# Optimization experiments

Measured on AMD Instinct MI355X. Metric: run time of the kernel, lower is better.

Reference implementation:

```python
import jax, jax.numpy as jnp
import numpy as np

F = 128
NRBF = 20
CUTOFF = 5.0
L = 3
NZ = 100
F2 = F // 2
N = 10000
E = 256000
NMOL = 100
EPS = 1e-8


def setup_inputs() -> dict:
    key = jax.random.key(0)
    ks = jax.random.split(key, 20)
    xyz = jax.random.uniform(ks[0], (N, 3), jnp.float32) * 10.0
    z = jax.random.randint(ks[1], (N,), 0, NZ)
    nbrs = jax.random.randint(ks[2], (E, 2), 0, N)
    # avoid self-edges (would give zero distance in the sinc RBF)
    nbrs = nbrs.at[:, 1].set(jnp.where(nbrs[:, 1] == nbrs[:, 0], (nbrs[:, 1] + 1) % N, nbrs[:, 1]))
    mol_idx = jnp.sort(jax.random.randint(ks[3], (N,), 0, NMOL))

    def p(k, shape, scale=0.05):
        return jax.random.normal(k, shape, jnp.float32) * scale

    return dict(
        xyz=xyz, z=z, nbrs=nbrs, mol_idx=mol_idx,
        emb=p(ks[4], (NZ, F), 1.0),
        msg_W1=p(ks[5], (L, F, F)), msg_b1=jnp.zeros((L, F), jnp.float32),
        msg_W2=p(ks[6], (L, F, 3 * F)), msg_b2=jnp.zeros((L, 3 * F), jnp.float32),
        dist_W=p(ks[7], (L, NRBF, 3 * F)), dist_b=jnp.zeros((L, 3 * F), jnp.float32),
        upd_U=p(ks[8], (L, F, F)), upd_V=p(ks[9], (L, F, F)),
        upd_W1=p(ks[10], (L, 2 * F, F)), upd_b1=jnp.zeros((L, F), jnp.float32),
        upd_W2=p(ks[11], (L, F, 3 * F)), upd_b2=jnp.zeros((L, 3 * F), jnp.float32),
        read_W1=p(ks[12], (F, F2)), read_b1=jnp.zeros((F2,), jnp.float32),
        read_W2=p(ks[13], (F2, 1)), read_b2=jnp.zeros((1,), jnp.float32),
    )


def _painn(xyz, emb, msg_W1, msg_b1, msg_W2, msg_b2, dist_W, dist_b,
           upd_U, upd_V, upd_W1, upd_b1, upd_W2, upd_b2,
           read_W1, read_b1, read_W2, read_b2, z, nbrs, mol_idx):
    idx_i = nbrs[:, 0]
    idx_j = nbrs[:, 1]
    r_ij = xyz[idx_j] - xyz[idx_i]                       # [E,3]
    d = jnp.sqrt(jnp.sum(r_ij * r_ij, -1) + EPS)          # [E]
    unit = r_ij / d[:, None]
    # sinc radial basis + cosine cutoff envelope
    nvec = jnp.arange(1, NRBF + 1, dtype=xyz.dtype)
    rbf = jnp.sin(nvec[None, :] * jnp.pi * d[:, None] / CUTOFF) / d[:, None]   # [E,NRBF]
    fcut = 0.5 * (jnp.cos(jnp.pi * d / CUTOFF) + 1.0) * (d < CUTOFF)           # [E]

    s_i = emb[z]                                          # [N,F]
    v_i = jnp.zeros((xyz.shape[0], F, 3), xyz.dtype)      # [N,F,3]

    for l in range(L):
        # message block: invariant filter on nodes, gather to edges
        phi = (jax.nn.silu(s_i @ msg_W1[l] + msg_b1[l]) @ msg_W2[l] + msg_b2[l])[idx_j]  # [E,3F]
        w_s = (rbf @ dist_W[l] + dist_b[l]) * fcut[:, None]                               # [E,3F]
        inv = (phi * w_s).reshape(-1, 3, F)
        ds_edge = inv[:, 0]                                                               # [E,F]
        dv_edge = inv[:, 1][:, :, None] * v_i[idx_j] + inv[:, 2][:, :, None] * unit[:, None, :]  # [E,F,3]
        s_i = s_i + jax.ops.segment_sum(ds_edge, idx_i, num_segments=s_i.shape[0])
        v_i = v_i + jax.ops.segment_sum(dv_edge, idx_i, num_segments=s_i.shape[0])

        # update block: channel-mixing of vectors + gated scalar/vector residuals
        u_v = jnp.einsum('nfv,fg->ngv', v_i, upd_U[l])
        v_v = jnp.einsum('nfv,fg->ngv', v_i, upd_V[l])
        vnorm = jnp.sqrt(jnp.sum(v_v * v_v, -1) + EPS)                                    # [N,F]
        a = (jax.nn.silu(jnp.concatenate([s_i, vnorm], -1) @ upd_W1[l] + upd_b1[l])
             @ upd_W2[l] + upd_b2[l]).reshape(-1, 3, F)
        dv = u_v * a[:, 0][:, :, None]
        ds = a[:, 1] * jnp.sum(u_v * v_v, -1) + a[:, 2]
        s_i = s_i + ds
        v_i = v_i + dv

    atom_e = jax.nn.silu(s_i @ read_W1 + read_b1) @ read_W2 + read_b2                     # [N,1]
    energy = jax.ops.segment_sum(atom_e[:, 0], mol_idx, num_segments=NMOL)                # [NMOL]
    return energy


def reference(xyz, z, nbrs, mol_idx, emb, msg_W1, msg_b1, msg_W2, msg_b2,
              dist_W, dist_b, upd_U, upd_V, upd_W1, upd_b1, upd_W2, upd_b2,
              read_W1, read_b1, read_W2, read_b2):
    return _painn(xyz, emb, msg_W1, msg_b1, msg_W2, msg_b2, dist_W, dist_b,
                  upd_U, upd_V, upd_W1, upd_b1, upd_W2, upd_b2,
                  read_W1, read_b1, read_W2, read_b2, z, nbrs, mol_idx)
```

## Files before the change

### kernel.cpp

```cpp
#include <hip/hip_runtime.h>
#include <hip/hip_bf16.h>
#include <math.h>

#define NA 10000
#define NE 256000
#define FDIM 128
#define F3 384
#define NRBF 20
#define NLAYERS 3
#define NMOLS 100
#define CAP 96
#define WROW 388
#define PACK_BLOCKS 2288
#define CUTOFF_F 5.0f
#define EPS_F 1e-8f
#define PI_F 3.14159265358979323846f

typedef __attribute__((ext_vector_type(8))) short bf16x8;
typedef __attribute__((ext_vector_type(4))) float f32x4;

struct pv6 { unsigned int u0, u1, u2; };

__device__ __forceinline__ float silu_f(float x) { return x / (1.0f + __expf(-x)); }

__device__ __forceinline__ unsigned short f2bf(float x) {
  unsigned u = __float_as_uint(x);
  return (unsigned short)((u + 0x7FFFu + ((u >> 16) & 1u)) >> 16);
}
__device__ __forceinline__ float bf2f(unsigned short u) {
  return __uint_as_float(((unsigned)u) << 16);
}
__device__ __forceinline__ float lo_f(unsigned int u) { return bf2f((unsigned short)(u & 0xFFFFu)); }
__device__ __forceinline__ float hi_f(unsigned int u) { return bf2f((unsigned short)(u >> 16)); }

__device__ __forceinline__ void pack_one(const float* __restrict__ src,
                                         unsigned short* __restrict__ dst,
                                         int loc, int per, int N) {
  int lay = loc / per;
  int kn = loc - lay * per;
  int k = kn / N, n = kn - k * N;
  int kb = k >> 5, q = (k >> 3) & 3, j = k & 7, nt = n >> 4, c = n & 15;
  int NT = N >> 4;
  dst[(size_t)lay * per + (((kb * NT + nt) * 64 + (q * 16 + c)) * 8 + j)] = f2bf(src[loc]);
}

__device__ __forceinline__ void pack_dw(const float* __restrict__ dW,
                                        const float* __restrict__ db,
                                        unsigned short* __restrict__ dst, int loc) {
  int lay = loc / 12288;
  int kn = loc - lay * 12288;
  int k = kn / 384, n = kn - k * 384;
  float val = 0.0f;
  if (k < NRBF) val = dW[lay * NRBF * 384 + k * 384 + n];
  else if (k == NRBF) val = db[lay * 384 + n];
  int q = (k >> 3) & 3, j = k & 7, nt = n >> 4, c = n & 15;
  dst[(size_t)lay * 12288 + ((nt * 64 + (q * 16 + c)) * 8 + j)] = f2bf(val);
}

__global__ __launch_bounds__(256) void prep_kernel(
    const float* __restrict__ msgW1, const float* __restrict__ msgW2,
    const float* __restrict__ updU, const float* __restrict__ updV,
    const float* __restrict__ updW1, const float* __restrict__ updW2,
    const float* __restrict__ rW1, const float* __restrict__ distW,
    const float* __restrict__ distb, unsigned short* __restrict__ dst,
    const float* __restrict__ xyz, const int* __restrict__ nbrs,
    float* __restrict__ unitv, unsigned short* __restrict__ rbf_bf,
    float* __restrict__ fcut,
    int* __restrict__ deg, int* __restrict__ slot_e, int* __restrict__ slot_j) {
  int b = blockIdx.x;
  if (b < PACK_BLOCKS) {
    int t = b * 256 + threadIdx.x;
    if (t < 49152) pack_one(msgW1, dst, t, 16384, 128);
    else if (t < 196608) pack_one(msgW2, dst + 49152, t - 49152, 49152, 384);
    else if (t < 245760) pack_one(updU, dst + 196608, t - 196608, 16384, 128);
    else if (t < 294912) pack_one(updV, dst + 245760, t - 245760, 16384, 128);
    else if (t < 393216) pack_one(updW1, dst + 294912, t - 294912, 32768, 128);
    else if (t < 540672) pack_one(updW2, dst + 393216, t - 393216, 49152, 384);
    else if (t < 548864) pack_one(rW1, dst + 540672, t - 540672, 8192, 64);
    else if (t < 585728) pack_dw(distW, distb, dst + 548864, t - 548864);
    return;
  }
  int e = (b - PACK_BLOCKS) * 256 + threadIdx.x;
  if (e >= NE) return;
  int i = nbrs[2 * e + 0], j = nbrs[2 * e + 1];
  float rx = xyz[3 * j + 0] - xyz[3 * i + 0];
  float ry = xyz[3 * j + 1] - xyz[3 * i + 1];
  float rz = xyz[3 * j + 2] - xyz[3 * i + 2];
  float d = sqrtf(rx * rx + ry * ry + rz * rz + EPS_F);
  if (d >= CUTOFF_F) return;
  float invd = 1.0f / d;
  float fc = 0.5f * (__cosf(PI_F * d / CUTOFF_F) + 1.0f);
  unitv[3 * e + 0] = rx * invd;
  unitv[3 * e + 1] = ry * invd;
  unitv[3 * e + 2] = rz * invd;
  fcut[e] = fc;
  float base = PI_F * d / CUTOFF_F;
  float sc = invd * fc;
#pragma unroll
  for (int k = 0; k < NRBF; k++)
    rbf_bf[(size_t)e * NRBF + k] = f2bf(__sinf((float)(k + 1) * base) * sc);
  int pos = atomicAdd(&deg[i], 1);
  if (pos < CAP) {
    slot_e[i * CAP + pos] = e;
    slot_j[i * CAP + pos] = j;
  }
}

__global__ __launch_bounds__(256) void msg0_mfma_kernel(
    const float* __restrict__ emb, const int* __restrict__ z, float* __restrict__ s_out,
    const unsigned short* __restrict__ pW1, const float* __restrict__ b1,
    const unsigned short* __restrict__ pW2, const float* __restrict__ b2,
    pv6* __restrict__ cmb) {
  __shared__ bf16x8 sA[4 * 64];
  __shared__ bf16x8 hA[4 * 64];
  int a0 = blockIdx.x * 16;
  int t = threadIdx.x;
  int lane = t & 63, w = t >> 6;
  {
    int kb = t >> 6, l = t & 63;
    int m = l & 15, q = l >> 4;
    int zi = z[a0 + m];
    const float* sp = emb + (size_t)zi * FDIM + kb * 32 + q * 8;
    float* so = s_out + (size_t)(a0 + m) * FDIM + kb * 32 + q * 8;
    bf16x8 c;
#pragma unroll
    for (int j = 0; j < 8; j++) {
      float v = sp[j];
      so[j] = v;
      c[j] = (short)f2bf(v);
    }
    sA[kb * 64 + l] = c;
  }
  __syncthreads();
  f32x4 accH[2];
#pragma unroll
  for (int t2 = 0; t2 < 2; t2++)
#pragma unroll
    for (int r = 0; r < 4; r++) accH[t2][r] = 0.0f;
  const bf16x8* W1f = (const bf16x8*)pW1;
#pragma unroll
  for (int kb = 0; kb < 4; kb++) {
    bf16x8 a = sA[kb * 64 + lane];
#pragma unroll
    for (int t2 = 0; t2 < 2; t2++) {
      bf16x8 b = W1f[(kb * 8 + 2 * w + t2) * 64 + lane];
      accH[t2] = __builtin_amdgcn_mfma_f32_16x16x32_bf16(a, b, accH[t2], 0, 0, 0);
    }
  }
  short* hs = (short*)hA;
#pragma unroll
  for (int t2 = 0; t2 < 2; t2++) {
    int n = w * 32 + t2 * 16 + (lane & 15);
    int kb = n >> 5, q = (n >> 3) & 3, j = n & 7;
    float bias = b1[n];
#pragma unroll
    for (int r = 0; r < 4; r++) {
      int m = (lane >> 4) * 4 + r;
      hs[(kb * 64 + q * 16 + m) * 8 + j] = (short)f2bf(silu_f(accH[t2][r] + bias));
    }
  }
  __syncthreads();
  f32x4 accP[3][2];
#pragma unroll
  for (int c3 = 0; c3 < 3; c3++)
#pragma unroll
    for (int t2 = 0; t2 < 2; t2++)
#pragma unroll
      for (int r = 0; r < 4; r++) accP[c3][t2][r] = 0.0f;
  const bf16x8* W2f = (const bf16x8*)pW2;
#pragma unroll
  for (int kb = 0; kb < 4; kb++) {
    bf16x8 a = hA[kb * 64 + lane];
#pragma unroll
    for (int c3 = 0; c3 < 3; c3++)
#pragma unroll
      for (int t2 = 0; t2 < 2; t2++) {
        bf16x8 b = W2f[(kb * 24 + c3 * 8 + 2 * w + t2) * 64 + lane];
        accP[c3][t2] = __builtin_amdgcn_mfma_f32_16x16x32_bf16(a, b, accP[c3][t2], 0, 0, 0);
      }
  }
#pragma unroll
  for (int t2 = 0; t2 < 2; t2++) {
    int g = (2 * w + t2) * 16 + (lane & 15);
    float bb0 = b2[g], bb1 = b2[FDIM + g], bb2 = b2[2 * FDIM + g];
#pragma unroll
    for (int r = 0; r < 4; r++) {
      int m = (lane >> 4) * 4 + r;
      unsigned p0 = f2bf(accP[0][t2][r] + bb0);
      unsigned p1 = f2bf(accP[1][t2][r] + bb1);
      unsigned p2 = f2bf(accP[2][t2][r] + bb2);
      pv6 rec;
      rec.u0 = p0 | (p1 << 16);
      rec.u1 = p2;
      rec.u2 = 0;
      cmb[(size_t)(a0 + m) * FDIM + g] = rec;
    }
  }
}

__global__ __launch_bounds__(128) void edge_kernel(
    const pv6* __restrict__ cmb, unsigned short* __restrict__ v_lin,
    float* __restrict__ s, const unsigned short* __restrict__ pDW,
    const int* __restrict__ deg, const int* __restrict__ slot_e,
    const int* __restrict__ slot_j, const unsigned short* __restrict__ rbf_bf,
    const float* __restrict__ fcut, const float* __restrict__ unitv) {
  __shared__ bf16x8 aLDS[64];
  __shared__ unsigned short w_lds[16][WROW];
  __shared__ float l_u[16][3];
  __shared__ int l_j[16];
  int i = blockIdx.x;
  int t = threadIdx.x;
  int f = t;
  int lane = t & 63, w = t >> 6;
  int cnt = deg[i];
  if (cnt > CAP) cnt = CAP;
  int base = i * CAP;
  float acc_s = 0.f, av0 = 0.f, av1 = 0.f, av2 = 0.f;
  const bf16x8* Bf = (const bf16x8*)pDW;
  for (int c0 = 0; c0 < cnt; c0 += 16) {
    int ccnt = cnt - c0;
    if (ccnt > 16) ccnt = 16;
    __syncthreads();
    if (t < 64) {
      int m = t & 15, q = t >> 4;
      bf16x8 a;
#pragma unroll
      for (int j = 0; j < 8; j++) a[j] = 0;
      int p = c0 + m;
      if (p < cnt) {
        int e = slot_e[base + p];
        const unsigned short* rb = rbf_bf + (size_t)e * NRBF;
#pragma unroll
        for (int j = 0; j < 8; j++) {
          int k = q * 8 + j;
          if (k < NRBF) a[j] = (short)rb[k];
          else if (k == NRBF) a[j] = (short)f2bf(fcut[e]);
        }
      }
      aLDS[t] = a;
    } else if (t < 80) {
      int idx = t - 64;
      int p = c0 + idx;
      if (p < cnt) {
        int e = slot_e[base + p];
        l_j[idx] = slot_j[base + p];
        l_u[idx][0] = unitv[3 * e + 0];
        l_u[idx][1] = unitv[3 * e + 1];
        l_u[idx][2] = unitv[3 * e + 2];
      }
    }
    __syncthreads();
    {
      bf16x8 a = aLDS[lane];
      int n0 = lane & 15, m0 = (lane >> 4) * 4;
#pragma unroll
      for (int tt = 0; tt < 12; tt++) {
        int nt = 12 * w + tt;
        f32x4 acc;
#pragma unroll
        for (int r = 0; r < 4; r++) acc[r] = 0.0f;
        acc = __builtin_amdgcn_mfma_f32_16x16x32_bf16(a, Bf[nt * 64 + lane], acc, 0, 0, 0);
        int n = nt * 16 + n0;
#pragma unroll
        for (int r = 0; r < 4; r++) w_lds[m0 + r][n] = f2bf(acc[r]);
      }
    }
    __syncthreads();
    int pp = 0;
    for (; pp + 4 <= ccnt; pp += 4) {
      pv6 R[4];
#pragma unroll
      for (int u = 0; u < 4; u++) R[u] = cmb[(size_t)l_j[pp + u] * FDIM + f];
#pragma unroll
      for (int u = 0; u < 4; u++) {
        float p0 = lo_f(R[u].u0), p1 = hi_f(R[u].u0), p2 = lo_f(R[u].u1);
        float v0 = hi_f(R[u].u1), v1 = lo_f(R[u].u2), v2 = hi_f(R[u].u2);
        float w0 = bf2f(w_lds[pp + u][f]), w1 = bf2f(w_lds[pp + u][FDIM + f]),
              w2 = bf2f(w_lds[pp + u][2 * FDIM + f]);
        acc_s += p0 * w0;
        float i1 = p1 * w1, i2 = p2 * w2;
        av0 += i1 * v0 + i2 * l_u[pp + u][0];
        av1 += i1 * v1 + i2 * l_u[pp + u][1];
        av2 += i1 * v2 + i2 * l_u[pp + u][2];
      }
    }
    for (; pp < ccnt; pp++) {
      pv6 R0 = cmb[(size_t)l_j[pp] * FDIM + f];
      float p0 = lo_f(R0.u0), p1 = hi_f(R0.u0), p2 = lo_f(R0.u1);
      float v0 = hi_f(R0.u1), v1 = lo_f(R0.u2), v2 = hi_f(R0.u2);
      float w0 = bf2f(w_lds[pp][f]), w1 = bf2f(w_lds[pp][FDIM + f]),
            w2 = bf2f(w_lds[pp][2 * FDIM + f]);
      acc_s += p0 * w0;
      float i1 = p1 * w1, i2 = p2 * w2;
      av0 += i1 * v0 + i2 * l_u[pp][0];
      av1 += i1 * v1 + i2 * l_u[pp][1];
      av2 += i1 * v2 + i2 * l_u[pp][2];
    }
  }
  {
    pv6 RI = cmb[(size_t)i * FDIM + f];
    av0 += hi_f(RI.u1);
    av1 += lo_f(RI.u2);
    av2 += hi_f(RI.u2);
  }
  unsigned short* vlo = v_lin + (size_t)i * F3;
  vlo[f] = f2bf(av0);
  vlo[FDIM + f] = f2bf(av1);
  vlo[2 * FDIM + f] = f2bf(av2);
  s[(size_t)i * FDIM + f] += acc_s;
}

__global__ __launch_bounds__(256) void upd_fused_kernel(
    float* __restrict__ s, const unsigned short* __restrict__ v_lin,
    pv6* __restrict__ cmb,
    const unsigned short* __restrict__ pU, const unsigned short* __restrict__ pV,
    const unsigned short* __restrict__ pW1, const float* __restrict__ b1,
    const unsigned short* __restrict__ pW2, const float* __restrict__ b2,
    int mode,
    const unsigned short* __restrict__ pMW1, const float* __restrict__ mb1,
    const unsigned short* __restrict__ pMW2, const float* __restrict__ mb2,
    const unsigned short* __restrict__ pRW1, const float* __restrict__ rb1,
    const float* __restrict__ rW2, const float* __restrict__ rb2,
    float* __restrict__ atom_e) {
  __shared__ bf16x8 vAf[3 * 4 * 64];
  __shared__ bf16x8 catA[8 * 64];
  __shared__ bf16x8 hA[4 * 64];
  __shared__ float red[4][16];
  int a0 = blockIdx.x * 16;
  int t = threadIdx.x;
  int lane = t & 63, w = t >> 6;
  {
    int l = t & 63, kb = (t >> 6) & 3;
    int m = l & 15, q = l >> 4;
#pragma unroll
    for (int rt = 0; rt < 3; rt++) {
      vAf[(rt * 4 + kb) * 64 + l] =
          *(const bf16x8*)(v_lin + (size_t)(a0 + m) * F3 + rt * FDIM + kb * 32 + q * 8);
    }
    const float* sp = s + (size_t)(a0 + m) * FDIM + kb * 32 + q * 8;
    bf16x8 c;
#pragma unroll
    for (int j = 0; j < 8; j++) c[j] = (short)f2bf(sp[j]);
    catA[kb * 64 + l] = c;
  }
  __syncthreads();
  f32x4 accU[3][2], accV[3][2];
#pragma unroll
  for (int rt = 0; rt < 3; rt++)
#pragma unroll
    for (int t2 = 0; t2 < 2; t2++)
#pragma unroll
      for (int r = 0; r < 4; r++) { accU[rt][t2][r] = 0.0f; accV[rt][t2][r] = 0.0f; }
  const bf16x8* Uf = (const bf16x8*)pU;
  const bf16x8* Vf = (const bf16x8*)pV;
#pragma unroll
  for (int kb = 0; kb < 4; kb++) {
    bf16x8 bu[2], bv[2];
#pragma unroll
    for (int t2 = 0; t2 < 2; t2++) {
      bu[t2] = Uf[(kb * 8 + 2 * w + t2) * 64 + lane];
      bv[t2] = Vf[(kb * 8 + 2 * w + t2) * 64 + lane];
    }
#pragma unroll
    for (int rt = 0; rt < 3; rt++) {
      bf16x8 a = vAf[(rt * 4 + kb) * 64 + lane];
#pragma unroll
      for (int t2 = 0; t2 < 2; t2++) {
        accU[rt][t2] = __builtin_amdgcn_mfma_f32_16x16x32_bf16(a, bu[t2], accU[rt][t2], 0, 0, 0);
        accV[rt][t2] = __builtin_amdgcn_mfma_f32_16x16x32_bf16(a, bv[t2], accV[rt][t2], 0, 0, 0);
      }
    }
  }
  short* cs = (short*)catA;
#pragma unroll
  for (int t2 = 0; t2 < 2; t2++) {
    int g = w * 32 + t2 * 16 + (lane & 15);
    int k = 128 + g;
    int kb = k >> 5, q = (k >> 3) & 3, j = k & 7;
#pragma unroll
    for (int r = 0; r < 4; r++) {
      int m = (lane >> 4) * 4 + r;
      float x0 = accV[0][t2][r], x1 = accV[1][t2][r], x2 = accV[2][t2][r];
      cs[(kb * 64 + q * 16 + m) * 8 + j] = (short)f2bf(sqrtf(x0 * x0 + x1 * x1 + x2 * x2 + EPS_F));
    }
  }
  __syncthreads();
  f32x4 accH[2];
#pragma unroll
  for (int t2 = 0; t2 < 2; t2++)
#pragma unroll
    for (int r = 0; r < 4; r++) accH[t2][r] = 0.0f;
  const bf16x8* W1f = (const bf16x8*)pW1;
#pragma unroll
  for (int kb = 0; kb < 8; kb++) {
    bf16x8 a = catA[kb * 64 + lane];
#pragma unroll
    for (int t2 = 0; t2 < 2; t2++) {
      bf16x8 b = W1f[(kb * 8 + 2 * w + t2) * 64 + lane];
      accH[t2] = __builtin_amdgcn_mfma_f32_16x16x32_bf16(a, b, accH[t2], 0, 0, 0);
    }
  }
  short* hs = (short*)hA;
#pragma unroll
  for (int t2 = 0; t2 < 2; t2++) {
    int n = w * 32 + t2 * 16 + (lane & 15);
    int kb = n >> 5, q = (n >> 3) & 3, j = n & 7;
    float bias = b1[n];
#pragma unroll
    for (int r = 0; r < 4; r++) {
      int m = (lane >> 4) * 4 + r;
      hs[(kb * 64 + q * 16 + m) * 8 + j] = (short)f2bf(silu_f(accH[t2][r] + bias));
    }
  }
  __syncthreads();
  f32x4 accA[3][2];
#pragma unroll
  for (int c3 = 0; c3 < 3; c3++)
#pragma unroll
    for (int t2 = 0; t2 < 2; t2++)
#pragma unroll
      for (int r = 0; r < 4; r++) accA[c3][t2][r] = 0.0f;
  const bf16x8* W2f = (const bf16x8*)pW2;
#pragma unroll
  for (int kb = 0; kb < 4; kb++) {
    bf16x8 a = hA[kb * 64 + lane];
#pragma unroll
    for (int c3 = 0; c3 < 3; c3++)
#pragma unroll
      for (int t2 = 0; t2 < 2; t2++) {
        bf16x8 b = W2f[(kb * 24 + c3 * 8 + 2 * w + t2) * 64 + lane];
        accA[c3][t2] = __builtin_amdgcn_mfma_f32_16x16x32_bf16(a, b, accA[c3][t2], 0, 0, 0);
      }
  }
  const short* vls = (const short*)vAf;
  unsigned short v0keep[2][4];
#pragma unroll
  for (int t2 = 0; t2 < 2; t2++) {
    int g = w * 32 + t2 * 16 + (lane & 15);
    float bb0 = b2[g], bb1 = b2[FDIM + g], bb2 = b2[2 * FDIM + g];
    int kb = g >> 5, q = (g >> 3) & 3, j = g & 7;
#pragma unroll
    for (int r = 0; r < 4; r++) {
      int m = (lane >> 4) * 4 + r;
      int n = a0 + m;
      float a0v = accA[0][t2][r] + bb0;
      float a1v = accA[1][t2][r] + bb1;
      float a2v = accA[2][t2][r] + bb2;
      float dot = accU[0][t2][r] * accV[0][t2][r] + accU[1][t2][r] * accV[1][t2][r] +
                  accU[2][t2][r] * accV[2][t2][r];
      float s_new = s[(size_t)n * FDIM + g] + a1v * dot + a2v;
      if (mode == 0) {
        s[(size_t)n * FDIM + g] = s_new;
        float nv[3];
#pragma unroll
        for (int c = 0; c < 3; c++) {
          float vold = bf2f((unsigned short)vls[(((c * 4 + kb) * 64) + (q * 16 + m)) * 8 + j]);
          nv[c] = vold + a0v * accU[c][t2][r];
        }
        v0keep[t2][r] = f2bf(nv[0]);
        cmb[(size_t)n * FDIM + g].u2 = (unsigned)f2bf(nv[1]) | ((unsigned)f2bf(nv[2]) << 16);
      }
      cs[(kb * 64 + q * 16 + m) * 8 + j] = (short)f2bf(s_new);
    }
  }
  __syncthreads();
  if (mode == 0) {
    f32x4 accH2[2];
#pragma unroll
    for (int t2 = 0; t2 < 2; t2++)
#pragma unroll
      for (int r = 0; r < 4; r++) accH2[t2][r] = 0.0f;
    const bf16x8* MW1f = (const bf16x8*)pMW1;
#pragma unroll
    for (int kb = 0; kb < 4; kb++) {
      bf16x8 a = catA[kb * 64 + lane];
#pragma unroll
      for (int t2 = 0; t2 < 2; t2++) {
        bf16x8 b = MW1f[(kb * 8 + 2 * w + t2) * 64 + lane];
        accH2[t2] = __builtin_amdgcn_mfma_f32_16x16x32_bf16(a, b, accH2[t2], 0, 0, 0);
      }
    }
#pragma unroll
    for (int t2 = 0; t2 < 2; t2++) {
      int n = w * 32 + t2 * 16 + (lane & 15);
      int kb = n >> 5, q = (n >> 3) & 3, j = n & 7;
      float bias = mb1[n];
#pragma unroll
      for (int r = 0; r < 4; r++) {
        int m = (lane >> 4) * 4 + r;
        hs[(kb * 64 + q * 16 + m) * 8 + j] = (short)f2bf(silu_f(accH2[t2][r] + bias));
      }
    }
    __syncthreads();
    f32x4 accP[3][2];
#pragma unroll
    for (int c3 = 0; c3 < 3; c3++)
#pragma unroll
      for (int t2 = 0; t2 < 2; t2++)
#pragma unroll
        for (int r = 0; r < 4; r++) accP[c3][t2][r] = 0.0f;
    const bf16x8* MW2f = (const bf16x8*)pMW2;
#pragma unroll
    for (int kb = 0; kb < 4; kb++) {
      bf16x8 a = hA[kb * 64 + lane];
#pragma unroll
      for (int c3 = 0; c3 < 3; c3++)
#pragma unroll
        for (int t2 = 0; t2 < 2; t2++) {
          bf16x8 b = MW2f[(kb * 24 + c3 * 8 + 2 * w + t2) * 64 + lane];
          accP[c3][t2] = __builtin_amdgcn_mfma_f32_16x16x32_bf16(a, b, accP[c3][t2], 0, 0, 0);
        }
    }
#pragma unroll
    for (int t2 = 0; t2 < 2; t2++) {
      int g = (2 * w + t2) * 16 + (lane & 15);
      float bb0 = mb2[g], bb1 = mb2[FDIM + g], bb2v = mb2[2 * FDIM + g];
#pragma unroll
      for (int r = 0; r < 4; r++) {
        int m = (lane >> 4) * 4 + r;
        unsigned p0 = f2bf(accP[0][t2][r] + bb0);
        unsigned p1 = f2bf(accP[1][t2][r] + bb1);
        unsigned p2 = f2bf(accP[2][t2][r] + bb2v);
        pv6* rec = &cmb[(size_t)(a0 + m) * FDIM + g];
        rec->u0 = p0 | (p1 << 16);
        rec->u1 = p2 | ((unsigned)v0keep[t2][r] << 16);
      }
    }
  } else {
    f32x4 acc;
#pragma unroll
    for (int r = 0; r < 4; r++) acc[r] = 0.0f;
    const bf16x8* RW1f = (const bf16x8*)pRW1;
#pragma unroll
    for (int kb = 0; kb < 4; kb++) {
      bf16x8 a = catA[kb * 64 + lane];
      bf16x8 b = RW1f[(kb * 4 + w) * 64 + lane];
      acc = __builtin_amdgcn_mfma_f32_16x16x32_bf16(a, b, acc, 0, 0, 0);
    }
    int col = w * 16 + (lane & 15);
    float bias = rb1[col], w2v = rW2[col];
    float val[4];
#pragma unroll
    for (int r = 0; r < 4; r++) val[r] = silu_f(acc[r] + bias) * w2v;
#pragma unroll
    for (int off = 1; off < 16; off <<= 1)
#pragma unroll
      for (int r = 0; r < 4; r++) val[r] += __shfl_xor(val[r], off, 64);
    if ((lane & 15) == 0) {
#pragma unroll
      for (int r = 0; r < 4; r++) red[w][(lane >> 4) * 4 + r] = val[r];
    }
    __syncthreads();
    if (t < 16) {
      atom_e[a0 + t] = red[0][t] + red[1][t] + red[2][t] + red[3][t] + rb2[0];
    }
  }
}

__global__ __launch_bounds__(256) void mol_reduce_kernel(
    const float* __restrict__ atom_e, const int* __restrict__ mol_idx,
    float* __restrict__ out) {
  __shared__ float molsum[NMOLS];
  int t = threadIdx.x;
  if (t < NMOLS) molsum[t] = 0.0f;
  __syncthreads();
  int n = blockIdx.x * 256 + t;
  if (n < NA) atomicAdd(&molsum[mol_idx[n]], atom_e[n]);
  __syncthreads();
  if (t < NMOLS && molsum[t] != 0.0f) atomicAdd(&out[t], molsum[t]);
}

extern "C" void kernel_launch(void* const* d_in, const int* in_sizes, int n_in,
                              void* d_out, int out_size, void* d_ws, size_t ws_size,
                              hipStream_t stream) {
  const float* xyz = (const float*)d_in[0];
  const int* z = (const int*)d_in[1];
  const int* nbrs = (const int*)d_in[2];
  const int* mol = (const int*)d_in[3];
  const float* emb = (const float*)d_in[4];
  const float* msgW1 = (const float*)d_in[5];
  const float* msgb1 = (const float*)d_in[6];
  const float* msgW2 = (const float*)d_in[7];
  const float* msgb2 = (const float*)d_in[8];
  const float* distW = (const float*)d_in[9];
  const float* distb = (const float*)d_in[10];
  const float* updU = (const float*)d_in[11];
  const float* updV = (const float*)d_in[12];
  const float* updW1 = (const float*)d_in[13];
  const float* updb1 = (const float*)d_in[14];
  const float* updW2 = (const float*)d_in[15];
  const float* updb2 = (const float*)d_in[16];
  const float* rW1 = (const float*)d_in[17];
  const float* rb1 = (const float*)d_in[18];
  const float* rW2 = (const float*)d_in[19];
  const float* rb2 = (const float*)d_in[20];

  float* ws = (float*)d_ws;
  float* s = ws;      ws += (size_t)NA * FDIM;
  float* fcut = ws;   ws += (size_t)NE;
  float* unitv = ws;  ws += (size_t)NE * 3;
  float* atom_e = ws; ws += (size_t)NA;
  int* deg = (int*)ws;
  int* slot_e = deg + NA;
  int* slot_j = slot_e + NA * CAP;
  unsigned short* pk = (unsigned short*)(((uintptr_t)(slot_j + NA * CAP) + 15) & ~(uintptr_t)15);
  unsigned short* pMsgW1 = pk;
  unsigned short* pMsgW2 = pMsgW1 + 49152;
  unsigned short* pUpdU  = pMsgW2 + 147456;
  unsigned short* pUpdV  = pUpdU + 49152;
  unsigned short* pUpdW1 = pUpdV + 49152;
  unsigned short* pUpdW2 = pUpdW1 + 98304;
  unsigned short* pRW1   = pUpdW2 + 147456;
  unsigned short* pDW    = pRW1 + 8192;
  unsigned short* rbf_bf = (unsigned short*)(((uintptr_t)(pDW + 36864) + 15) & ~(uintptr_t)15);
  unsigned short* after_rbf = rbf_bf + (size_t)NE * NRBF + 8;
  pv6* cmb = (pv6*)(((uintptr_t)after_rbf + 15) & ~(uintptr_t)15);
  unsigned short* v_lin = (unsigned short*)(cmb + (size_t)NA * FDIM);

  hipMemsetAsync(deg, 0, NA * sizeof(int), stream);
  hipMemsetAsync(d_out, 0, NMOLS * sizeof(float), stream);

  prep_kernel<<<PACK_BLOCKS + NE / 256, 256, 0, stream>>>(
      msgW1, msgW2, updU, updV, updW1, updW2, rW1, distW, distb, pMsgW1,
      xyz, nbrs, unitv, rbf_bf, fcut, deg, slot_e, slot_j);
  msg0_mfma_kernel<<<NA / 16, 256, 0, stream>>>(emb, z, s, pMsgW1, msgb1, pMsgW2, msgb2, cmb);

  for (int l = 0; l < NLAYERS; l++) {
    edge_kernel<<<NA, 128, 0, stream>>>(cmb, v_lin, s,
                                        pDW + (size_t)l * 12288,
                                        deg, slot_e, slot_j, rbf_bf, fcut, unitv);
    int mode = (l == NLAYERS - 1) ? 1 : 0;
    int lnext = (l + 1 < NLAYERS) ? l + 1 : 0;
    upd_fused_kernel<<<NA / 16, 256, 0, stream>>>(
        s, v_lin, cmb, pUpdU + (size_t)l * 16384, pUpdV + (size_t)l * 16384,
        pUpdW1 + (size_t)l * 32768, updb1 + (size_t)l * FDIM,
        pUpdW2 + (size_t)l * 49152, updb2 + (size_t)l * F3,
        mode,
        pMsgW1 + (size_t)lnext * 16384, msgb1 + (size_t)lnext * FDIM,
        pMsgW2 + (size_t)lnext * 49152, msgb2 + (size_t)lnext * F3,
        pRW1, rb1, rW2, rb2, atom_e);
  }
  mol_reduce_kernel<<<(NA + 255) / 256, 256, 0, stream>>>(atom_e, mol, (float*)d_out);
}
```

Measured before the change: 298.9 us.

## Prefetch neighbor gathers across MFMA stage and cut barriers in edge kernel

The edge kernel now preloads all slot edge and neighbor indices into LDS once per atom. For each 16-edge chunk it issues all 16 neighbor record gathers up front, so they overlap the RBF MFMA that builds the filter weights. Each wave builds its own MFMA A-operand in registers instead of staging it through LDS, and the full __syncthreads calls are replaced by an lgkmcnt-wait plus s_barrier. The cost is more registers (16 pv6 records per thread), which the added launch bound of 4 has to accommodate, with some risk of spilling.

After: 402.2 us. +34.6%, slower.

```diff
diff --git a/kernel.cpp b/kernel.cpp
--- a/kernel.cpp
+++ b/kernel.cpp
@@ -32,6 +32,11 @@
 }
 __device__ __forceinline__ float lo_f(unsigned int u) { return bf2f((unsigned short)(u & 0xFFFFu)); }
 __device__ __forceinline__ float hi_f(unsigned int u) { return bf2f((unsigned short)(u >> 16)); }
+
+__device__ __forceinline__ void bar_lds() {
+  asm volatile("s_waitcnt lgkmcnt(0)" ::: "memory");
+  __builtin_amdgcn_s_barrier();
+}
 
 __device__ __forceinline__ void pack_one(const float* __restrict__ src,
                                          unsigned short* __restrict__ dst,
@@ -198,16 +203,16 @@
   }
 }
 
-__global__ __launch_bounds__(128) void edge_kernel(
+__global__ __launch_bounds__(128, 4) void edge_kernel(
     const pv6* __restrict__ cmb, unsigned short* __restrict__ v_lin,
     float* __restrict__ s, const unsigned short* __restrict__ pDW,
     const int* __restrict__ deg, const int* __restrict__ slot_e,
     const int* __restrict__ slot_j, const unsigned short* __restrict__ rbf_bf,
     const float* __restrict__ fcut, const float* __restrict__ unitv) {
-  __shared__ bf16x8 aLDS[64];
   __shared__ unsigned short w_lds[16][WROW];
   __shared__ float l_u[16][3];
-  __shared__ int l_j[16];
+  __shared__ int l_e_all[CAP];
+  __shared__ int l_j_all[CAP];
   int i = blockIdx.x;
   int t = threadIdx.x;
   int f = t;
@@ -215,20 +220,38 @@
   int cnt = deg[i];
   if (cnt > CAP) cnt = CAP;
   int base = i * CAP;
+  if (t < cnt) {
+    l_e_all[t] = slot_e[base + t];
+    l_j_all[t] = slot_j[base + t];
+  }
+  __syncthreads();
   float acc_s = 0.f, av0 = 0.f, av1 = 0.f, av2 = 0.f;
   const bf16x8* Bf = (const bf16x8*)pDW;
   for (int c0 = 0; c0 < cnt; c0 += 16) {
     int ccnt = cnt - c0;
     if (ccnt > 16) ccnt = 16;
-    __syncthreads();
-    if (t < 64) {
-      int m = t & 15, q = t >> 4;
-      bf16x8 a;
-#pragma unroll
-      for (int j = 0; j < 8; j++) a[j] = 0;
+    pv6 R[16];
+#pragma unroll
+    for (int u = 0; u < 16; u++)
+      if (c0 + u < cnt) R[u] = cmb[(size_t)l_j_all[c0 + u] * FDIM + f];
+    bar_lds();
+    if (t >= 64 && t < 80) {
+      int idx = t - 64, p = c0 + idx;
+      if (p < cnt) {
+        int e = l_e_all[p];
+        l_u[idx][0] = unitv[3 * e + 0];
+        l_u[idx][1] = unitv[3 * e + 1];
+        l_u[idx][2] = unitv[3 * e + 2];
+      }
+    }
+    bf16x8 a;
+#pragma unroll
+    for (int j = 0; j < 8; j++) a[j] = 0;
+    {
+      int m = lane & 15, q = lane >> 4;
       int p = c0 + m;
       if (p < cnt) {
-        int e = slot_e[base + p];
+        int e = l_e_all[p];
         const unsigned short* rb = rbf_bf + (size_t)e * NRBF;
 #pragma unroll
         for (int j = 0; j < 8; j++) {
@@ -237,21 +260,8 @@
           else if (k == NRBF) a[j] = (short)f2bf(fcut[e]);
         }
       }
-      aLDS[t] = a;
-    } else if (t < 80) {
-      int idx = t - 64;
-      int p = c0 + idx;
-      if (p < cnt) {
-        int e = slot_e[base + p];
-        l_j[idx] = slot_j[base + p];
-        l_u[idx][0] = unitv[3 * e + 0];
-        l_u[idx][1] = unitv[3 * e + 1];
-        l_u[idx][2] = unitv[3 * e + 2];
-      }
-    }
-    __syncthreads();
+    }
     {
-      bf16x8 a = aLDS[lane];
       int n0 = lane & 15, m0 = (lane >> 4) * 4;
 #pragma unroll
       for (int tt = 0; tt < 12; tt++) {
@@ -265,36 +275,20 @@
         for (int r = 0; r < 4; r++) w_lds[m0 + r][n] = f2bf(acc[r]);
       }
     }
-    __syncthreads();
-    int pp = 0;
-    for (; pp + 4 <= ccnt; pp += 4) {
-      pv6 R[4];
-#pragma unroll
-      for (int u = 0; u < 4; u++) R[u] = cmb[(size_t)l_j[pp + u] * FDIM + f];
-#pragma unroll
-      for (int u = 0; u < 4; u++) {
+    bar_lds();
+#pragma unroll
+    for (int u = 0; u < 16; u++) {
+      if (u < ccnt) {
         float p0 = lo_f(R[u].u0), p1 = hi_f(R[u].u0), p2 = lo_f(R[u].u1);
         float v0 = hi_f(R[u].u1), v1 = lo_f(R[u].u2), v2 = hi_f(R[u].u2);
-        float w0 = bf2f(w_lds[pp + u][f]), w1 = bf2f(w_lds[pp + u][FDIM + f]),
-              w2 = bf2f(w_lds[pp + u][2 * FDIM + f]);
+        float w0 = bf2f(w_lds[u][f]), w1 = bf2f(w_lds[u][FDIM + f]),
+              w2 = bf2f(w_lds[u][2 * FDIM + f]);
         acc_s += p0 * w0;
         float i1 = p1 * w1, i2 = p2 * w2;
-        av0 += i1 * v0 + i2 * l_u[pp + u][0];
-        av1 += i1 * v1 + i2 * l_u[pp + u][1];
-        av2 += i1 * v2 + i2 * l_u[pp + u][2];
-      }
-    }
-    for (; pp < ccnt; pp++) {
-      pv6 R0 = cmb[(size_t)l_j[pp] * FDIM + f];
-      float p0 = lo_f(R0.u0), p1 = hi_f(R0.u0), p2 = lo_f(R0.u1);
-      float v0 = hi_f(R0.u1), v1 = lo_f(R0.u2), v2 = hi_f(R0.u2);
-      float w0 = bf2f(w_lds[pp][f]), w1 = bf2f(w_lds[pp][FDIM + f]),
-            w2 = bf2f(w_lds[pp][2 * FDIM + f]);
-      acc_s += p0 * w0;
-      float i1 = p1 * w1, i2 = p2 * w2;
-      av0 += i1 * v0 + i2 * l_u[pp][0];
-      av1 += i1 * v1 + i2 * l_u[pp][1];
-      av2 += i1 * v2 + i2 * l_u[pp][2];
+        av0 += i1 * v0 + i2 * l_u[u][0];
+        av1 += i1 * v1 + i2 * l_u[u][1];
+        av2 += i1 * v2 + i2 * l_u[u][2];
+      }
     }
   }
   {
```

## Split edge aggregation into per-16-edge chunk blocks with atomic accumulation

Applied to the files above, without the earlier changes.

The per-atom edge kernel, which looped over up to 96 neighbours in 16-edge chunks, is replaced by a grid of NA*6 blocks that each handle one 16-edge chunk and atomically add their scalar and vector contributions into global fp32 buffers. The vector state now lives in an fp32 v_acc buffer that the update kernel reads, converts to bf16, and rewrites with the residual-updated values, so the self-term no longer needs to be added in the edge kernel. The goal is more parallelism and shorter per-block serial chains. The cost is a zeroing memset, many early-exiting empty blocks, four fp32 atomics per thread per chunk, and double the vector storage traffic from using fp32.

After: 315.4 us. 1.06x slower.

```diff
diff --git a/kernel.cpp b/kernel.cpp
--- a/kernel.cpp
+++ b/kernel.cpp
@@ -10,6 +10,7 @@
 #define NLAYERS 3
 #define NMOLS 100
 #define CAP 96
+#define MAXCH 6
 #define WROW 388
 #define PACK_BLOCKS 2288
 #define CUTOFF_F 5.0f
@@ -198,120 +199,109 @@
   }
 }
 
-__global__ __launch_bounds__(128) void edge_kernel(
-    const pv6* __restrict__ cmb, unsigned short* __restrict__ v_lin,
+__global__ __launch_bounds__(128) void edge_chunk_kernel(
+    const pv6* __restrict__ cmb, float* __restrict__ v_acc,
     float* __restrict__ s, const unsigned short* __restrict__ pDW,
     const int* __restrict__ deg, const int* __restrict__ slot_e,
     const int* __restrict__ slot_j, const unsigned short* __restrict__ rbf_bf,
     const float* __restrict__ fcut, const float* __restrict__ unitv) {
-  __shared__ bf16x8 aLDS[64];
-  __shared__ unsigned short w_lds[16][WROW];
+  __shared__ __align__(16) unsigned short w_lds[16][WROW];
   __shared__ float l_u[16][3];
+  __shared__ int l_e[16];
   __shared__ int l_j[16];
-  int i = blockIdx.x;
-  int t = threadIdx.x;
-  int f = t;
-  int lane = t & 63, w = t >> 6;
+  int b = blockIdx.x;
+  int i = b % NA, c = b / NA;
+  int off = c * 16;
   int cnt = deg[i];
   if (cnt > CAP) cnt = CAP;
-  int base = i * CAP;
+  if (off >= cnt) return;
+  int ccnt = cnt - off;
+  if (ccnt > 16) ccnt = 16;
+  int t = threadIdx.x;
+  int lane = t & 63, w = t >> 6;
+  int base = i * CAP + off;
+  if (t < 16) {
+    int p = base + (t < ccnt ? t : 0);
+    int e = slot_e[p];
+    l_e[t] = e;
+    l_j[t] = slot_j[p];
+    l_u[t][0] = unitv[3 * e + 0];
+    l_u[t][1] = unitv[3 * e + 1];
+    l_u[t][2] = unitv[3 * e + 2];
+  }
+  __syncthreads();
+  int m16 = lane & 15, q4 = lane >> 4;
+  bf16x8 a;
+#pragma unroll
+  for (int j = 0; j < 8; j++) a[j] = 0;
+  if (q4 < 3 && m16 < ccnt) {
+    int e = l_e[m16];
+    const unsigned short* rb = rbf_bf + (size_t)e * NRBF;
+    if (q4 < 2) {
+#pragma unroll
+      for (int j = 0; j < 8; j++) a[j] = (short)rb[q4 * 8 + j];
+    } else {
+#pragma unroll
+      for (int j = 0; j < 4; j++) a[j] = (short)rb[16 + j];
+      a[4] = (short)f2bf(fcut[e]);
+    }
+  }
+  const bf16x8* Bf = (const bf16x8*)pDW;
+  {
+    int mrow = q4 * 4;
+#pragma unroll
+    for (int tt = 0; tt < 12; tt++) {
+      int nt = 12 * w + tt;
+      f32x4 acc;
+#pragma unroll
+      for (int r = 0; r < 4; r++) acc[r] = 0.0f;
+      acc = __builtin_amdgcn_mfma_f32_16x16x32_bf16(a, Bf[nt * 64 + lane], acc, 0, 0, 0);
+      int n = nt * 16 + m16;
+#pragma unroll
+      for (int r = 0; r < 4; r++) w_lds[mrow + r][n] = f2bf(acc[r]);
+    }
+  }
+  __syncthreads();
+  int f = t;
   float acc_s = 0.f, av0 = 0.f, av1 = 0.f, av2 = 0.f;
-  const bf16x8* Bf = (const bf16x8*)pDW;
-  for (int c0 = 0; c0 < cnt; c0 += 16) {
-    int ccnt = cnt - c0;
-    if (ccnt > 16) ccnt = 16;
-    __syncthreads();
-    if (t < 64) {
-      int m = t & 15, q = t >> 4;
-      bf16x8 a;
-#pragma unroll
-      for (int j = 0; j < 8; j++) a[j] = 0;
-      int p = c0 + m;
-      if (p < cnt) {
-        int e = slot_e[base + p];
-        const unsigned short* rb = rbf_bf + (size_t)e * NRBF;
-#pragma unroll
-        for (int j = 0; j < 8; j++) {
-          int k = q * 8 + j;
-          if (k < NRBF) a[j] = (short)rb[k];
-          else if (k == NRBF) a[j] = (short)f2bf(fcut[e]);
-        }
-      }
-      aLDS[t] = a;
-    } else if (t < 80) {
-      int idx = t - 64;
-      int p = c0 + idx;
-      if (p < cnt) {
-        int e = slot_e[base + p];
-        l_j[idx] = slot_j[base + p];
-        l_u[idx][0] = unitv[3 * e + 0];
-        l_u[idx][1] = unitv[3 * e + 1];
-        l_u[idx][2] = unitv[3 * e + 2];
-      }
-    }
-    __syncthreads();
-    {
-      bf16x8 a = aLDS[lane];
-      int n0 = lane & 15, m0 = (lane >> 4) * 4;
-#pragma unroll
-      for (int tt = 0; tt < 12; tt++) {
-        int nt = 12 * w + tt;
-        f32x4 acc;
-#pragma unroll
-        for (int r = 0; r < 4; r++) acc[r] = 0.0f;
-        acc = __builtin_amdgcn_mfma_f32_16x16x32_bf16(a, Bf[nt * 64 + lane], acc, 0, 0, 0);
-        int n = nt * 16 + n0;
-#pragma unroll
-        for (int r = 0; r < 4; r++) w_lds[m0 + r][n] = f2bf(acc[r]);
-      }
-    }
-    __syncthreads();
-    int pp = 0;
-    for (; pp + 4 <= ccnt; pp += 4) {
-      pv6 R[4];
-#pragma unroll
-      for (int u = 0; u < 4; u++) R[u] = cmb[(size_t)l_j[pp + u] * FDIM + f];
-#pragma unroll
-      for (int u = 0; u < 4; u++) {
-        float p0 = lo_f(R[u].u0), p1 = hi_f(R[u].u0), p2 = lo_f(R[u].u1);
-        float v0 = hi_f(R[u].u1), v1 = lo_f(R[u].u2), v2 = hi_f(R[u].u2);
-        float w0 = bf2f(w_lds[pp + u][f]), w1 = bf2f(w_lds[pp + u][FDIM + f]),
-              w2 = bf2f(w_lds[pp + u][2 * FDIM + f]);
-        acc_s += p0 * w0;
-        float i1 = p1 * w1, i2 = p2 * w2;
-        av0 += i1 * v0 + i2 * l_u[pp + u][0];
-        av1 += i1 * v1 + i2 * l_u[pp + u][1];
-        av2 += i1 * v2 + i2 * l_u[pp + u][2];
-      }
-    }
-    for (; pp < ccnt; pp++) {
-      pv6 R0 = cmb[(size_t)l_j[pp] * FDIM + f];
-      float p0 = lo_f(R0.u0), p1 = hi_f(R0.u0), p2 = lo_f(R0.u1);
-      float v0 = hi_f(R0.u1), v1 = lo_f(R0.u2), v2 = hi_f(R0.u2);
-      float w0 = bf2f(w_lds[pp][f]), w1 = bf2f(w_lds[pp][FDIM + f]),
-            w2 = bf2f(w_lds[pp][2 * FDIM + f]);
+  int pp = 0;
+  for (; pp + 4 <= ccnt; pp += 4) {
+    pv6 R[4];
+#pragma unroll
+    for (int u = 0; u < 4; u++) R[u] = cmb[(size_t)l_j[pp + u] * FDIM + f];
+#pragma unroll
+    for (int u = 0; u < 4; u++) {
+      float p0 = lo_f(R[u].u0), p1 = hi_f(R[u].u0), p2 = lo_f(R[u].u1);
+      float v0 = hi_f(R[u].u1), v1 = lo_f(R[u].u2), v2 = hi_f(R[u].u2);
+      float w0 = bf2f(w_lds[pp + u][f]), w1 = bf2f(w_lds[pp + u][FDIM + f]),
+            w2 = bf2f(w_lds[pp + u][2 * FDIM + f]);
       acc_s += p0 * w0;
       float i1 = p1 * w1, i2 = p2 * w2;
-      av0 += i1 * v0 + i2 * l_u[pp][0];
-      av1 += i1 * v1 + i2 * l_u[pp][1];
-      av2 += i1 * v2 + i2 * l_u[pp][2];
-    }
-  }
-  {
-    pv6 RI = cmb[(size_t)i * FDIM + f];
-    av0 += hi_f(RI.u1);
-    av1 += lo_f(RI.u2);
-    av2 += hi_f(RI.u2);
-  }
-  unsigned short* vlo = v_lin + (size_t)i * F3;
-  vlo[f] = f2bf(av0);
-  vlo[FDIM + f] = f2bf(av1);
-  vlo[2 * FDIM + f] = f2bf(av2);
-  s[(size_t)i * FDIM + f] += acc_s;
+      av0 += i1 * v0 + i2 * l_u[pp + u][0];
+      av1 += i1 * v1 + i2 * l_u[pp + u][1];
+      av2 += i1 * v2 + i2 * l_u[pp + u][2];
+    }
+  }
+  for (; pp < ccnt; pp++) {
+    pv6 R0 = cmb[(size_t)l_j[pp] * FDIM + f];
+    float p0 = lo_f(R0.u0), p1 = hi_f(R0.u0), p2 = lo_f(R0.u1);
+    float v0 = hi_f(R0.u1), v1 = lo_f(R0.u2), v2 = hi_f(R0.u2);
+    float w0 = bf2f(w_lds[pp][f]), w1 = bf2f(w_lds[pp][FDIM + f]),
+          w2 = bf2f(w_lds[pp][2 * FDIM + f]);
+    acc_s += p0 * w0;
+    float i1 = p1 * w1, i2 = p2 * w2;
+    av0 += i1 * v0 + i2 * l_u[pp][0];
+    av1 += i1 * v1 + i2 * l_u[pp][1];
+    av2 += i1 * v2 + i2 * l_u[pp][2];
+  }
+  atomicAdd(&s[(size_t)i * FDIM + f], acc_s);
+  atomicAdd(&v_acc[((size_t)i * 3 + 0) * FDIM + f], av0);
+  atomicAdd(&v_acc[((size_t)i * 3 + 1) * FDIM + f], av1);
+  atomicAdd(&v_acc[((size_t)i * 3 + 2) * FDIM + f], av2);
 }
 
 __global__ __launch_bounds__(256) void upd_fused_kernel(
-    float* __restrict__ s, const unsigned short* __restrict__ v_lin,
+    float* __restrict__ s, float* __restrict__ v_acc,
     pv6* __restrict__ cmb,
     const unsigned short* __restrict__ pU, const unsigned short* __restrict__ pV,
     const unsigned short* __restrict__ pW1, const float* __restrict__ b1,
@@ -334,8 +324,16 @@
     int m = l & 15, q = l >> 4;
 #pragma unroll
     for (int rt = 0; rt < 3; rt++) {
-      vAf[(rt * 4 + kb) * 64 + l] =
-          *(const bf16x8*)(v_lin + (size_t)(a0 + m) * F3 + rt * FDIM + kb * 32 + q * 8);
+      const float* vp = v_acc + ((size_t)(a0 + m) * 3 + rt) * FDIM + kb * 32 + q * 8;
+      f32x4 va = *(const f32x4*)vp;
+      f32x4 vb = *(const f32x4*)(vp + 4);
+      bf16x8 cvv;
+#pragma unroll
+      for (int j = 0; j < 4; j++) {
+        cvv[j] = (short)f2bf(va[j]);
+        cvv[4 + j] = (short)f2bf(vb[j]);
+      }
+      vAf[(rt * 4 + kb) * 64 + l] = cvv;
     }
     const float* sp = s + (size_t)(a0 + m) * FDIM + kb * 32 + q * 8;
     bf16x8 c;
@@ -459,6 +457,9 @@
         }
         v0keep[t2][r] = f2bf(nv[0]);
         cmb[(size_t)n * FDIM + g].u2 = (unsigned)f2bf(nv[1]) | ((unsigned)f2bf(nv[2]) << 16);
+        v_acc[((size_t)n * 3 + 0) * FDIM + g] = nv[0];
+        v_acc[((size_t)n * 3 + 1) * FDIM + g] = nv[1];
+        v_acc[((size_t)n * 3 + 2) * FDIM + g] = nv[2];
       }
       cs[(kb * 64 + q * 16 + m) * 8 + j] = (short)f2bf(s_new);
     }
@@ -615,9 +616,10 @@
   unsigned short* rbf_bf = (unsigned short*)(((uintptr_t)(pDW + 36864) + 15) & ~(uintptr_t)15);
   unsigned short* after_rbf = rbf_bf + (size_t)NE * NRBF + 8;
   pv6* cmb = (pv6*)(((uintptr_t)after_rbf + 15) & ~(uintptr_t)15);
-  unsigned short* v_lin = (unsigned short*)(cmb + (size_t)NA * FDIM);
+  float* v_acc = (float*)(cmb + (size_t)NA * FDIM);
 
   hipMemsetAsync(deg, 0, NA * sizeof(int), stream);
+  hipMemsetAsync(v_acc, 0, (size_t)NA * F3 * sizeof(float), stream);
   hipMemsetAsync(d_out, 0, NMOLS * sizeof(float), stream);
 
   prep_kernel<<<PACK_BLOCKS + NE / 256, 256, 0, stream>>>(
@@ -626,13 +628,13 @@
   msg0_mfma_kernel<<<NA / 16, 256, 0, stream>>>(emb, z, s, pMsgW1, msgb1, pMsgW2, msgb2, cmb);
 
   for (int l = 0; l < NLAYERS; l++) {
-    edge_kernel<<<NA, 128, 0, stream>>>(cmb, v_lin, s,
-                                        pDW + (size_t)l * 12288,
-                                        deg, slot_e, slot_j, rbf_bf, fcut, unitv);
+    edge_chunk_kernel<<<NA * MAXCH, 128, 0, stream>>>(
+        cmb, v_acc, s, pDW + (size_t)l * 12288,
+        deg, slot_e, slot_j, rbf_bf, fcut, unitv);
     int mode = (l == NLAYERS - 1) ? 1 : 0;
     int lnext = (l + 1 < NLAYERS) ? l + 1 : 0;
     upd_fused_kernel<<<NA / 16, 256, 0, stream>>>(
-        s, v_lin, cmb, pUpdU + (size_t)l * 16384, pUpdV + (size_t)l * 16384,
+        s, v_acc, cmb, pUpdU + (size_t)l * 16384, pUpdV + (size_t)l * 16384,
         pUpdW1 + (size_t)l * 32768, updb1 + (size_t)l * FDIM,
         pUpdW2 + (size_t)l * 49152, updb2 + (size_t)l * F3,
         mode,
```
